# Kernel tuning notes

Hardware: AMD Instinct MI355X
Metric: run time of the kernel (lower is better)

The kernel has to match this reference:

```python
import jax, jax.numpy as jnp
import numpy as np

B, S, H = 32, 512, 768
V = 8192
W_MAX = 256  # max words per sample after merging subwords


def setup_inputs() -> dict:
    key = jax.random.key(0)
    k1, k2, k3 = jax.random.split(key, 3)
    bert_encodings = jax.random.normal(k1, (B, S, H), dtype=jnp.float32)
    # per-token word index, sorted per row -> contiguous ragged segments
    segment_ids = jnp.sort(jax.random.randint(k2, (B, S), 0, W_MAX, dtype=jnp.int32), axis=1)
    W = jax.random.normal(k3, (H, V), dtype=jnp.float32) * 0.02
    b = jnp.zeros((V,), dtype=jnp.float32)
    return {
        "bert_encodings": bert_encodings,
        "segment_ids": segment_ids,
        "W": W,
        "b": b,
        "num_words": W_MAX,
    }


def reference(bert_encodings, segment_ids, W, b, num_words):
    Bb, Ss, Hh = bert_encodings.shape
    # Flatten batch: give each sample its own block of segment ids so one
    # segment_sum handles the whole batch (fused segment-reduce).
    flat_ids = (segment_ids + jnp.arange(Bb, dtype=segment_ids.dtype)[:, None] * num_words).reshape(-1)
    flat_enc = bert_encodings.reshape(-1, Hh)
    sums = jax.ops.segment_sum(flat_enc, flat_ids, num_segments=Bb * num_words)  # [B*W, H]
    counts = jax.ops.segment_sum(jnp.ones((Bb * Ss,), dtype=flat_enc.dtype), flat_ids,
                                 num_segments=Bb * num_words)  # [B*W]
    # mean per word; words with no subwords are zero-padded (like pad_sequence)
    denom = jnp.where(counts > 0, counts, 1.0)[:, None]
    merged = jnp.where(counts[:, None] > 0, sums / denom, 0.0).reshape(Bb, num_words, Hh)
    logits = jnp.einsum("bwh,hv->bwv", merged, W) + b  # [B, W_MAX, V]
    return logits
```

## Files before the change

kernel.cpp:

```cpp
#include <hip/hip_runtime.h>
#include <cstdint>
#include <cstddef>

typedef unsigned short ushort_t;
typedef __bf16 bf16x8 __attribute__((ext_vector_type(8)));
typedef float f32x4 __attribute__((ext_vector_type(4)));
typedef float f32x4v __attribute__((ext_vector_type(4)));
typedef unsigned short u16x4 __attribute__((ext_vector_type(4)));
typedef unsigned short u16x8 __attribute__((ext_vector_type(8)));

__device__ __forceinline__ ushort_t f2bf(float x) {
    union { float f; uint32_t u; } v; v.f = x;
    return (ushort_t)((v.u + 0x7FFFu + ((v.u >> 16) & 1u)) >> 16);
}

__device__ __forceinline__ void gld_lds16(const void* g, void* l) {
    __builtin_amdgcn_global_load_lds(
        (const __attribute__((address_space(1))) uint32_t*)g,
        (__attribute__((address_space(3))) uint32_t*)l,
        16, 0, 0);
}

__global__ __launch_bounds__(256) void transpose_convert(
    const float* __restrict__ Wm, ushort_t* __restrict__ Wt, int H, int V)
{
    __shared__ ushort_t tile[64][72];
    const int v0 = blockIdx.x * 64;
    const int k0 = blockIdx.y * 64;
    const int tid = threadIdx.x;

    #pragma unroll
    for (int p = 0; p < 4; ++p) {
        const int krow = p * 16 + (tid >> 4);
        const int vcol = (tid & 15) * 4;
        const f32x4v w = *(const f32x4v*)&Wm[(size_t)(k0 + krow) * V + v0 + vcol];
        tile[vcol + 0][krow] = f2bf(w.x);
        tile[vcol + 1][krow] = f2bf(w.y);
        tile[vcol + 2][krow] = f2bf(w.z);
        tile[vcol + 3][krow] = f2bf(w.w);
    }
    __syncthreads();
    #pragma unroll
    for (int p = 0; p < 2; ++p) {
        const int idx = p * 256 + tid;
        const int v = idx >> 3;
        const int c = (idx & 7) * 8;
        const u16x8 val = *(const u16x8*)&tile[v][c];
        *(u16x8*)&Wt[(size_t)(v0 + v) * H + k0 + c] = val;
    }
}

__global__ __launch_bounds__(256) void seg_mean(
    const float* __restrict__ enc,
    const int*   __restrict__ seg,
    ushort_t*    __restrict__ merged,
    int S, int H, int W)
{
    const int wave = threadIdx.x >> 6;
    const int lane = threadIdx.x & 63;
    const int bw = blockIdx.x * 4 + wave;
    const int b  = bw >> 8;
    const int w  = bw & 255;
    const int* srow = seg + (size_t)b * S;

    int l = 0, r = S;
    while (l < r) { int m = (l + r) >> 1; if (srow[m] < w) l = m + 1; else r = m; }
    const int lo = l;
    r = S;
    while (l < r) { int m = (l + r) >> 1; if (srow[m] < w + 1) l = m + 1; else r = m; }
    const int hi = l;

    const int cnt = hi - lo;
    const float scale = (cnt > 0) ? (1.0f / (float)cnt) : 0.0f;
    const float* erow = enc + (size_t)b * S * H;
    ushort_t* orow = merged + (size_t)bw * H;

    #pragma unroll
    for (int c = 0; c < 3; ++c) {
        const int col = c * 256 + lane * 4;
        f32x4v s = {0.f, 0.f, 0.f, 0.f};
        for (int t = lo; t < hi; ++t) {
            const f32x4v v = *(const f32x4v*)&erow[(size_t)t * H + col];
            s.x += v.x; s.y += v.y; s.z += v.z; s.w += v.w;
        }
        u16x4 o;
        o.x = f2bf(s.x * scale); o.y = f2bf(s.y * scale);
        o.z = f2bf(s.z * scale); o.w = f2bf(s.w * scale);
        *(u16x4*)&orow[col] = o;
    }
}

__global__ __launch_bounds__(256) void gemm_bt(
    const ushort_t* __restrict__ A,
    const ushort_t* __restrict__ Bt,
    const float*    __restrict__ bias,
    float*          __restrict__ C,
    int M, int N, int K)
{
    __shared__ ushort_t As[2][128 * 32];
    __shared__ ushort_t Bs[2][128 * 32];

    const int tid  = threadIdx.x;
    const int wave = tid >> 6;
    const int lane = tid & 63;
    const int wm   = wave >> 1;
    const int wn   = wave & 1;
    const int r15  = lane & 15;
    const int quad = lane >> 4;

    const int m0 = blockIdx.y * 128;
    const int n0 = blockIdx.x * 128;

    const int srow = tid >> 2;
    const int scol = (tid & 3) * 8;

    const ushort_t* Ag = A  + (size_t)(m0 + srow) * K + scol;
    const ushort_t* Bg = Bt + (size_t)(n0 + srow) * K + scol;
    const int wofs = wave * 512;

    f32x4 acc[4][4] = {};

    const int a_fo = (wm * 64 + r15) * 32 + quad * 8;
    const int b_fo = (wn * 64 + r15) * 32 + quad * 8;

    for (int kt = 0; kt < K; kt += 64) {
        gld_lds16(Ag + kt,                        &As[0][wofs]);
        gld_lds16(Ag + (size_t)64 * K + kt,       &As[0][wofs + 2048]);
        gld_lds16(Bg + kt,                        &Bs[0][wofs]);
        gld_lds16(Bg + (size_t)64 * K + kt,       &Bs[0][wofs + 2048]);
        gld_lds16(Ag + kt + 32,                   &As[1][wofs]);
        gld_lds16(Ag + (size_t)64 * K + kt + 32,  &As[1][wofs + 2048]);
        gld_lds16(Bg + kt + 32,                   &Bs[1][wofs]);
        gld_lds16(Bg + (size_t)64 * K + kt + 32,  &Bs[1][wofs + 2048]);
        __syncthreads();

        #pragma unroll
        for (int h = 0; h < 2; ++h) {
            bf16x8 af[4], bf[4];
            #pragma unroll
            for (int i = 0; i < 4; ++i) {
                af[i] = *(const bf16x8*)(&As[h][a_fo + i * 16 * 32]);
                bf[i] = *(const bf16x8*)(&Bs[h][b_fo + i * 16 * 32]);
            }
            #pragma unroll
            for (int i = 0; i < 4; ++i)
                #pragma unroll
                for (int j = 0; j < 4; ++j)
                    acc[i][j] = __builtin_amdgcn_mfma_f32_16x16x32_bf16(
                                    af[i], bf[j], acc[i][j], 0, 0, 0);
        }
        __syncthreads();
    }

    const int crow = m0 + wm * 64 + quad * 4;
    const int ccol = n0 + wn * 64 + r15;
    #pragma unroll
    for (int j = 0; j < 4; ++j) {
        const float bv = bias[ccol + j * 16];
        #pragma unroll
        for (int i = 0; i < 4; ++i) {
            float* cp = C + (size_t)(crow + i * 16) * N + (ccol + j * 16);
            #pragma unroll
            for (int r = 0; r < 4; ++r)
                cp[(size_t)r * N] = acc[i][j][r] + bv;
        }
    }
}

extern "C" void kernel_launch(void* const* d_in, const int* in_sizes, int n_in,
                              void* d_out, int out_size, void* d_ws, size_t ws_size,
                              hipStream_t stream) {
    const float* enc  = (const float*)d_in[0];
    const int*   seg  = (const int*)d_in[1];
    const float* Wm   = (const float*)d_in[2];
    const float* bias = (const float*)d_in[3];

    const int B = 32, S = 512, H = 768, V = 8192, WMAX = 256;
    const int M = B * WMAX;

    ushort_t* Wt     = (ushort_t*)d_ws;
    ushort_t* merged = Wt + (size_t)V * H;
    float*    out    = (float*)d_out;

    hipLaunchKernelGGL(transpose_convert, dim3(V / 64, H / 64), dim3(256), 0, stream,
                       Wm, Wt, H, V);
    hipLaunchKernelGGL(seg_mean, dim3(M / 4), dim3(256), 0, stream,
                       enc, seg, merged, S, H, WMAX);
    hipLaunchKernelGGL(gemm_bt, dim3(V / 128, M / 128), dim3(256), 0, stream,
                       merged, Wt, bias, out, M, V, H);
}
```

Baseline: 452.9 us.

## Replace GEMM with 256x256-tile, 8-wave pipelined kernel using swizzled LDS

Swaps the 128x128 4-wave GEMM for a 256x256 tile kernel with 512 threads. It stages A and B halves into double-buffered, XOR-swizzled LDS, interleaving prefetch of the next k-tiles with MFMA phases across barriers. It also uses s_setprio around MFMA bursts and a grouped block-index remap for L2 locality. The goal is more data reuse per loaded byte, fewer LDS bank conflicts and overlap of loads with compute. The cost is heavier register and LDS use and a more fragile schedule.

```diff
diff --git a/kernel.cpp b/kernel.cpp
--- a/kernel.cpp
+++ b/kernel.cpp
@@ -90,79 +90,147 @@
     }
 }
 
-__global__ __launch_bounds__(256) void gemm_bt(
+
+#define BAR() do { asm volatile("" ::: "memory"); \
+                   __builtin_amdgcn_s_barrier(); \
+                   asm volatile("" ::: "memory"); } while (0)
+
+#define STG_A(U, S) do { \
+    const ushort_t* g_ = Ag + (U) * 64 + (size_t)(S) * 64 * K; \
+    char* l_ = ldsA + ((((U) & 1) * 2 + (S)) * 16384); \
+    gld_lds16(g_, l_); \
+    gld_lds16(g_ + (size_t)128 * K, l_ + 8192); \
+} while (0)
+
+#define STG_B(U, S) do { \
+    const ushort_t* g_ = Bg + (U) * 64 + (size_t)(S) * 32 * K; \
+    char* l_ = ldsB + ((((U) & 1) * 2 + (S)) * 16384); \
+    gld_lds16(g_, l_); \
+    gld_lds16(g_ + (size_t)128 * K, l_ + 8192); \
+} while (0)
+
+#define LDA(DST, MS, I, KK) \
+    DST = *(const bf16x8*)(Ar + cur * 32768 + (MS) * 16384 + \
+          (wm * 64 + (I) * 16 + r15) * 128 + (((KK) * 64 + quad * 16) ^ rswz))
+
+#define LDB(DST, NS, J, KK) \
+    DST = *(const bf16x8*)(Br + cur * 32768 + (NS) * 16384 + \
+          (wn * 32 + (J) * 16 + r15) * 128 + (((KK) * 64 + quad * 16) ^ rswz))
+
+#define MFMA_PH(MS, NS, BF) do { \
+    __builtin_amdgcn_s_setprio(1); \
+    _Pragma("unroll") \
+    for (int i_ = 0; i_ < 4; ++i_) { \
+      _Pragma("unroll") \
+      for (int j_ = 0; j_ < 2; ++j_) { \
+        acc[MS][i_][NS][j_] = __builtin_amdgcn_mfma_f32_16x16x32_bf16( \
+            af[i_][0], BF[j_][0], acc[MS][i_][NS][j_], 0, 0, 0); \
+        acc[MS][i_][NS][j_] = __builtin_amdgcn_mfma_f32_16x16x32_bf16( \
+            af[i_][1], BF[j_][1], acc[MS][i_][NS][j_], 0, 0, 0); \
+      } \
+    } \
+    __builtin_amdgcn_s_setprio(0); \
+} while (0)
+
+__global__ __launch_bounds__(512, 2) void gemm_bt256(
     const ushort_t* __restrict__ A,
     const ushort_t* __restrict__ Bt,
     const float*    __restrict__ bias,
     float*          __restrict__ C,
     int M, int N, int K)
 {
-    __shared__ ushort_t As[2][128 * 32];
-    __shared__ ushort_t Bs[2][128 * 32];
+    __shared__ ushort_t As[2][2][8192];
+    __shared__ ushort_t Bs[2][2][8192];
 
     const int tid  = threadIdx.x;
     const int wave = tid >> 6;
     const int lane = tid & 63;
-    const int wm   = wave >> 1;
-    const int wn   = wave & 1;
     const int r15  = lane & 15;
     const int quad = lane >> 4;
-
-    const int m0 = blockIdx.y * 128;
-    const int n0 = blockIdx.x * 128;
-
-    const int srow = tid >> 2;
-    const int scol = (tid & 3) * 8;
-
-    const ushort_t* Ag = A  + (size_t)(m0 + srow) * K + scol;
-    const ushort_t* Bg = Bt + (size_t)(n0 + srow) * K + scol;
-    const int wofs = wave * 512;
-
-    f32x4 acc[4][4] = {};
-
-    const int a_fo = (wm * 64 + r15) * 32 + quad * 8;
-    const int b_fo = (wn * 64 + r15) * 32 + quad * 8;
-
-    for (int kt = 0; kt < K; kt += 64) {
-        gld_lds16(Ag + kt,                        &As[0][wofs]);
-        gld_lds16(Ag + (size_t)64 * K + kt,       &As[0][wofs + 2048]);
-        gld_lds16(Bg + kt,                        &Bs[0][wofs]);
-        gld_lds16(Bg + (size_t)64 * K + kt,       &Bs[0][wofs + 2048]);
-        gld_lds16(Ag + kt + 32,                   &As[1][wofs]);
-        gld_lds16(Ag + (size_t)64 * K + kt + 32,  &As[1][wofs + 2048]);
-        gld_lds16(Bg + kt + 32,                   &Bs[1][wofs]);
-        gld_lds16(Bg + (size_t)64 * K + kt + 32,  &Bs[1][wofs + 2048]);
-        __syncthreads();
-
-        #pragma unroll
-        for (int h = 0; h < 2; ++h) {
-            bf16x8 af[4], bf[4];
+    const int wm   = wave >> 2;
+    const int wn   = wave & 3;
+    const int rswz = (r15 & 7) << 4;
+
+    const int wg  = blockIdx.x;
+    const int swz = (wg & 7) * 128 + (wg >> 3);
+    const int m0  = (swz >> 5) * 256;
+    const int n0  = (swz & 31) * 256;
+
+    const int rho0 = tid >> 3;
+    const int cBb  = (tid & 7) * 16;
+    const int colA = (cBb ^ ((rho0 & 7) << 4)) >> 1;
+    const int grB0 = ((rho0 >> 5) << 6) + (rho0 & 31);
+
+    const ushort_t* Ag = A  + (size_t)(m0 + rho0) * K + colA;
+    const ushort_t* Bg = Bt + (size_t)(n0 + grB0) * K + colA;
+    char* ldsA = (char*)As + wave * 1024;
+    char* ldsB = (char*)Bs + wave * 1024;
+    const char* Ar = (const char*)As;
+    const char* Br = (const char*)Bs;
+
+    const int T = K >> 6;
+
+    f32x4 acc[2][4][2][2] = {};
+
+    STG_A(0, 0); STG_B(0, 0); STG_A(0, 1); STG_B(0, 1);
+    STG_A(1, 0); STG_B(1, 0);
+    asm volatile("s_waitcnt vmcnt(4)" ::: "memory");
+    BAR();
+
+    bf16x8 af[4][2], bf0[2][2], bf1[2][2];
+
+    for (int t = 0; t < T; ++t) {
+        const int cur = t & 1;
+        int u1 = t + 1; if (u1 >= T) u1 = t - 1;
+        int u2 = t + 2; if (u2 >= T) u2 = t;
+
+        #pragma unroll
+        for (int i = 0; i < 4; ++i) { LDA(af[i][0], 0, i, 0); LDA(af[i][1], 0, i, 1); }
+        #pragma unroll
+        for (int j = 0; j < 2; ++j) { LDB(bf0[j][0], 0, j, 0); LDB(bf0[j][1], 0, j, 1); }
+        STG_A(u1, 1);
+        BAR();
+        MFMA_PH(0, 0, bf0);
+        BAR();
+
+        #pragma unroll
+        for (int j = 0; j < 2; ++j) { LDB(bf1[j][0], 1, j, 0); LDB(bf1[j][1], 1, j, 1); }
+        STG_B(u1, 1);
+        BAR();
+        MFMA_PH(0, 1, bf1);
+        BAR();
+
+        #pragma unroll
+        for (int i = 0; i < 4; ++i) { LDA(af[i][0], 1, i, 0); LDA(af[i][1], 1, i, 1); }
+        STG_A(u2, 0);
+        BAR();
+        MFMA_PH(1, 0, bf0);
+        BAR();
+
+        STG_B(u2, 0);
+        BAR();
+        MFMA_PH(1, 1, bf1);
+        asm volatile("s_waitcnt vmcnt(4)" ::: "memory");
+        BAR();
+    }
+
+    #pragma unroll
+    for (int ms = 0; ms < 2; ++ms) {
+        #pragma unroll
+        for (int i = 0; i < 4; ++i) {
+            const int row = m0 + wm * 128 + ms * 64 + i * 16 + quad * 4;
             #pragma unroll
-            for (int i = 0; i < 4; ++i) {
-                af[i] = *(const bf16x8*)(&As[h][a_fo + i * 16 * 32]);
-                bf[i] = *(const bf16x8*)(&Bs[h][b_fo + i * 16 * 32]);
+            for (int ns = 0; ns < 2; ++ns) {
+                #pragma unroll
+                for (int j = 0; j < 2; ++j) {
+                    const int col = n0 + wn * 64 + ns * 32 + j * 16 + r15;
+                    const float bv = bias[col];
+                    float* cp = C + (size_t)row * N + col;
+                    #pragma unroll
+                    for (int r = 0; r < 4; ++r)
+                        cp[(size_t)r * N] = acc[ms][i][ns][j][r] + bv;
+                }
             }
-            #pragma unroll
-            for (int i = 0; i < 4; ++i)
-                #pragma unroll
-                for (int j = 0; j < 4; ++j)
-                    acc[i][j] = __builtin_amdgcn_mfma_f32_16x16x32_bf16(
-                                    af[i], bf[j], acc[i][j], 0, 0, 0);
-        }
-        __syncthreads();
-    }
-
-    const int crow = m0 + wm * 64 + quad * 4;
-    const int ccol = n0 + wn * 64 + r15;
-    #pragma unroll
-    for (int j = 0; j < 4; ++j) {
-        const float bv = bias[ccol + j * 16];
-        #pragma unroll
-        for (int i = 0; i < 4; ++i) {
-            float* cp = C + (size_t)(crow + i * 16) * N + (ccol + j * 16);
-            #pragma unroll
-            for (int r = 0; r < 4; ++r)
-                cp[(size_t)r * N] = acc[i][j][r] + bv;
         }
     }
 }
@@ -186,6 +254,6 @@
                        Wm, Wt, H, V);
     hipLaunchKernelGGL(seg_mean, dim3(M / 4), dim3(256), 0, stream,
                        enc, seg, merged, S, H, WMAX);
-    hipLaunchKernelGGL(gemm_bt, dim3(V / 128, M / 128), dim3(256), 0, stream,
+    hipLaunchKernelGGL(gemm_bt256, dim3((M / 256) * (V / 256)), dim3(512), 0, stream,
                        merged, Wt, bias, out, M, V, H);
 }
```

New measurement: 427.5 us. 1.06x faster.
